# Optimization experiments

Measured on AMD Instinct MI355X. Metric: run time of the kernel, lower is better.

Reference implementation:

```python
import jax, jax.numpy as jnp
import numpy as np

TOP_K = 2
LN_EPS = 1e-5
GATE_EPS = 1e-6


def setup_inputs() -> dict:
    key = jax.random.key(0)
    ks = jax.random.split(key, 5)
    B, D, E, H, O = 16384, 1200, 8, 1024, 1
    x = jax.random.normal(ks[0], (B, D), dtype=jnp.float32)
    w_gate = jax.random.normal(ks[1], (D, E), dtype=jnp.float32) * 0.05
    W1 = jax.random.normal(ks[2], (E, D, H), dtype=jnp.float32) * (1.0 / np.sqrt(D))
    b1 = jnp.zeros((E, H), dtype=jnp.float32)
    g1 = jnp.ones((E, H), dtype=jnp.float32)   # LayerNorm weight
    be1 = jnp.zeros((E, H), dtype=jnp.float32)  # LayerNorm bias
    W2 = jax.random.normal(ks[3], (E, H, O), dtype=jnp.float32) * (1.0 / np.sqrt(H))
    b2 = jnp.zeros((E, O), dtype=jnp.float32)
    return {"x": x, "w_gate": w_gate, "W1": W1, "b1": b1, "g1": g1, "be1": be1, "W2": W2, "b2": b2}


def reference(x, w_gate, W1, b1, g1, be1, W2, b2):
    B = x.shape[0]
    # --- top-k gating (eval mode: no noise) ---
    probs = jax.nn.softmax(x @ w_gate, axis=1)                 # [B, E]
    top_vals, top_idx = jax.lax.top_k(probs, TOP_K)            # [B, k]
    top_gates = top_vals / (jnp.sum(top_vals, axis=1, keepdims=True) + GATE_EPS)
    gates = jnp.zeros_like(probs).at[jnp.arange(B)[:, None], top_idx].set(top_gates)  # [B, E]
    # --- per-expert MLP (computed densely for all experts; gates zero out non-selected) ---
    h = jnp.einsum('bd,edh->beh', x, W1) + b1                  # [B, E, H]
    mu = jnp.mean(h, axis=-1, keepdims=True)
    var = jnp.var(h, axis=-1, keepdims=True)
    h = (h - mu) * jax.lax.rsqrt(var + LN_EPS) * g1 + be1      # LayerNorm
    h = jax.nn.relu(h)
    out = jax.nn.sigmoid(jnp.einsum('beh,eho->beo', h, W2) + b2)  # [B, E, O]
    # --- scatter/combine: weighted sum over experts ---
    y = jnp.einsum('be,beo->bo', gates, out)                   # [B, O]
    return y
```

## Files before the change

### kernel.cpp

```cpp
#include <hip/hip_runtime.h>
#include <hip/hip_bf16.h>
#include <stdint.h>

#define B_ROWS 16384
#define D_IN   1200
#define D_PAD  1216
#define N_EXP  8
#define H_DIM  1024
#define R_CAP  4608
#define CAP    36864
#define N_RT   288
#define LN_EPS 1e-5f
#define GATE_EPS 1e-6f
#define CNT_STRIDE 16

#define O_CNT    0
#define O_PROWC  512
#define O_PGATEC 147968
#define O_XBF    295424
#define O_W1T    40143744
#define O_HBUF   60066688

#define GATING_BLOCKS (B_ROWS / 16)
#define W1T_BLOCKS    (19 * 16 * 8)
#define PREP_BLOCKS   (GATING_BLOCKS + 1 + W1T_BLOCKS)

#define NT        (D_PAD / 32)

typedef short bf16x8 __attribute__((ext_vector_type(8)));
typedef short short8 __attribute__((ext_vector_type(8)));
typedef short short4v __attribute__((ext_vector_type(4)));
typedef float f32x4 __attribute__((ext_vector_type(4)));

__device__ __forceinline__ void load_lds16(const void* gptr, void* ldsptr) {
    __builtin_amdgcn_global_load_lds(
        (__attribute__((address_space(1))) void*)const_cast<void*>(gptr),
        (__attribute__((address_space(3))) void*)ldsptr, 16, 0, 0);
}

__device__ __forceinline__ short4v pack_bf16x4(float4 a) {
    union { short4v v; __hip_bfloat16 h[4]; } u;
    u.h[0] = __float2bfloat16(a.x); u.h[1] = __float2bfloat16(a.y);
    u.h[2] = __float2bfloat16(a.z); u.h[3] = __float2bfloat16(a.w);
    return u.v;
}

__global__ __launch_bounds__(256) void prep_kernel(
    const float* __restrict__ x, const float* __restrict__ wg,
    int* __restrict__ cnt, int* __restrict__ pairRowC, float* __restrict__ pairGateC,
    __hip_bfloat16* __restrict__ xbf, float* __restrict__ y,
    const float* __restrict__ W1, __hip_bfloat16* __restrict__ w1t)
{
    __shared__ int lcnt[N_EXP];
    __shared__ int base[N_EXP];
    __shared__ float tile[2][32][33];
    int bx = blockIdx.x;
    int tid = threadIdx.x;

    if (bx > GATING_BLOCKS) {
        int b = bx - GATING_BLOCKS - 1;
        int d0 = (b % 19) * 64;
        int h0 = ((b / 19) % 16) * 64;
        int e = b / (19 * 16);
        const float* src = W1 + (long)e * D_IN * H_DIM;

        int hs = tid & 15;
        int dr = tid >> 4;
#pragma unroll
        for (int s = 0; s < 4; ++s) {
            int dl = dr + 16 * s;
            int d = d0 + dl;
            float4 v = (d < D_IN)
                ? ((const float4*)(src + (long)d * H_DIM + h0))[hs]
                : (float4){0.f, 0.f, 0.f, 0.f};
            int drl = dl & 31;
            int hl = hs * 4;
            int Th = hl >> 5;
            int hh = hl & 31;
            tile[Th][drl][hh + 0] = v.x;
            tile[Th][drl][hh + 1] = v.y;
            tile[Th][drl][hh + 2] = v.z;
            tile[Th][drl][hh + 3] = v.w;
            if (s == 1) {
                __syncthreads();
                int T2 = tid >> 7, rr = tid & 127;
                int hl2 = rr >> 2, dseg = rr & 3;
                float f[8];
#pragma unroll
                for (int jj = 0; jj < 8; ++jj) f[jj] = tile[T2][dseg * 8 + jj][hl2];
                union { short8 v8; __hip_bfloat16 hh8[8]; } u;
#pragma unroll
                for (int jj = 0; jj < 8; ++jj) u.hh8[jj] = __float2bfloat16(f[jj]);
                int h = h0 + T2 * 32 + hl2;
                ((short8*)(w1t + (long)e * H_DIM * D_PAD + (long)h * D_PAD + d0))[dseg] = u.v8;
                __syncthreads();
            }
        }
        __syncthreads();
        {
            int T2 = tid >> 7, rr = tid & 127;
            int hl2 = rr >> 2, dseg = rr & 3;
            float f[8];
#pragma unroll
            for (int jj = 0; jj < 8; ++jj) f[jj] = tile[T2][dseg * 8 + jj][hl2];
            union { short8 v8; __hip_bfloat16 hh8[8]; } u;
#pragma unroll
            for (int jj = 0; jj < 8; ++jj) u.hh8[jj] = __float2bfloat16(f[jj]);
            int h = h0 + T2 * 32 + hl2;
            ((short8*)(w1t + (long)e * H_DIM * D_PAD + (long)h * D_PAD + d0 + 32))[dseg] = u.v8;
        }
        return;
    }

    if (bx == GATING_BLOCKS) {
        short8* xrow = (short8*)(xbf + (long)B_ROWS * D_PAD);
        if (tid < 152) xrow[tid] = (short8){0, 0, 0, 0, 0, 0, 0, 0};
        return;
    }

    if (tid < N_EXP) lcnt[tid] = 0;
    if (tid < 16) y[bx * 16 + tid] = 0.f;
    __syncthreads();

    int widx = tid >> 6;
    int lane = tid & 63;
    int rowbase = bx * 16 + widx * 4;
    const float* xw = x + (long)rowbase * D_IN;

    float acc[4][8];
#pragma unroll
    for (int r = 0; r < 4; ++r)
#pragma unroll
        for (int e = 0; e < N_EXP; ++e) acc[r][e] = 0.f;

    for (int i = lane; i < 304; i += 64) {
        if (i < 300) {
            const float4* wv4 = (const float4*)(wg + (long)i * 32);
            float4 w0 = wv4[0], w1v = wv4[1], w2 = wv4[2], w3 = wv4[3],
                   w4 = wv4[4], w5 = wv4[5], w6 = wv4[6], w7 = wv4[7];
#pragma unroll
            for (int r = 0; r < 4; ++r) {
                float4 xv = ((const float4*)(xw + (long)r * D_IN))[i];
                acc[r][0] += xv.x * w0.x + xv.y * w2.x + xv.z * w4.x + xv.w * w6.x;
                acc[r][1] += xv.x * w0.y + xv.y * w2.y + xv.z * w4.y + xv.w * w6.y;
                acc[r][2] += xv.x * w0.z + xv.y * w2.z + xv.z * w4.z + xv.w * w6.z;
                acc[r][3] += xv.x * w0.w + xv.y * w2.w + xv.z * w4.w + xv.w * w6.w;
                acc[r][4] += xv.x * w1v.x + xv.y * w3.x + xv.z * w5.x + xv.w * w7.x;
                acc[r][5] += xv.x * w1v.y + xv.y * w3.y + xv.z * w5.y + xv.w * w7.y;
                acc[r][6] += xv.x * w1v.z + xv.y * w3.z + xv.z * w5.z + xv.w * w7.z;
                acc[r][7] += xv.x * w1v.w + xv.y * w3.w + xv.z * w5.w + xv.w * w7.w;
                ((short4v*)(xbf + (long)(rowbase + r) * D_PAD))[i] = pack_bf16x4(xv);
            }
        } else {
#pragma unroll
            for (int r = 0; r < 4; ++r)
                ((short4v*)(xbf + (long)(rowbase + r) * D_PAD))[i] = (short4v){0, 0, 0, 0};
        }
    }

#pragma unroll
    for (int r = 0; r < 4; ++r)
#pragma unroll
        for (int e = 0; e < N_EXP; ++e) {
            float v = acc[r][e];
#pragma unroll
            for (int off = 32; off > 0; off >>= 1) v += __shfl_xor(v, off, 64);
            acc[r][e] = v;
        }

    float my[N_EXP];
#pragma unroll
    for (int e = 0; e < N_EXP; ++e) my[e] = acc[0][e];
#pragma unroll
    for (int r = 1; r < 4; ++r)
#pragma unroll
        for (int e = 0; e < N_EXP; ++e)
            if (lane == r) my[e] = acc[r][e];

    int i0 = 0, i1 = 1, s0 = 0, s1 = 0;
    float g0 = 0.f, g1 = 0.f;
    if (lane < 4) {
        float m = my[0];
#pragma unroll
        for (int e = 1; e < N_EXP; ++e) m = fmaxf(m, my[e]);
        float p[N_EXP], s = 0.f;
#pragma unroll
        for (int e = 0; e < N_EXP; ++e) { p[e] = expf(my[e] - m); s += p[e]; }
#pragma unroll
        for (int e = 1; e < N_EXP; ++e) if (p[e] > p[i0]) i0 = e;
        i1 = (i0 == 0) ? 1 : 0;
#pragma unroll
        for (int e = 0; e < N_EXP; ++e) if (e != i0 && p[e] > p[i1]) i1 = e;
        float v0 = p[i0] / s, v1 = p[i1] / s;
        float inv = 1.f / (v0 + v1 + GATE_EPS);
        g0 = v0 * inv; g1 = v1 * inv;
        s0 = atomicAdd(&lcnt[i0], 1);
        s1 = atomicAdd(&lcnt[i1], 1);
    }
    __syncthreads();
    if (tid < N_EXP) base[tid] = atomicAdd(&cnt[tid * CNT_STRIDE], lcnt[tid]);
    __syncthreads();
    if (lane < 4) {
        int row = rowbase + lane;
        int p0 = i0 * R_CAP + base[i0] + s0;
        pairRowC[p0] = row; pairGateC[p0] = g0;
        int p1 = i1 * R_CAP + base[i1] + s1;
        pairRowC[p1] = row; pairGateC[p1] = g1;
    }
}

__global__ __launch_bounds__(256) void gemm_kernel(
    const __hip_bfloat16* __restrict__ xbf, const __hip_bfloat16* __restrict__ w1t,
    const float* __restrict__ b1, const int* __restrict__ cnt,
    const int* __restrict__ pairRowC,
    __hip_bfloat16* __restrict__ hbuf)
{
    int bi = blockIdx.x;
    int xcd = bi & 7;
    int j = bi >> 3;
    int col0 = (j & 7) << 7;
    int rt = xcd * 36 + (j >> 3);
    int row0 = rt << 7;
    int e = xcd;
    int cnt_e = cnt[e * CNT_STRIDE];
    if (row0 - e * R_CAP >= cnt_e) return;

    __shared__ short lA[128 * 32];
    __shared__ short lB[128 * 32];

    int t = threadIdx.x;
    int lane = t & 63, w = t >> 6;
    int wm = (w >> 1) * 64, wn = (w & 1) * 64;
    int l15 = lane & 15, quad = lane >> 4;
    int qsw = quad ^ ((l15 >> 1) & 3);

    f32x4 acc[4][4];
#pragma unroll
    for (int i = 0; i < 4; ++i)
#pragma unroll
        for (int j2 = 0; j2 < 4; ++j2) acc[i][j2] = (f32x4){0.f, 0.f, 0.f, 0.f};

    int r1 = t >> 2, seg = t & 3;
    int sw = seg ^ ((r1 >> 1) & 3);
    int ridx1 = pairRowC[row0 + r1];
    int ridx2 = pairRowC[row0 + 64 + r1];
    ridx1 = ((unsigned)ridx1 > B_ROWS) ? B_ROWS : ridx1;
    ridx2 = ((unsigned)ridx2 > B_ROWS) ? B_ROWS : ridx2;
    const __hip_bfloat16* Arow1 = xbf + (long)ridx1 * D_PAD + sw * 8;
    const __hip_bfloat16* Arow2 = xbf + (long)ridx2 * D_PAD + sw * 8;
    const __hip_bfloat16* Bb = w1t + (long)e * H_DIM * D_PAD + (long)col0 * D_PAD;
    const __hip_bfloat16* Brow1 = Bb + (long)r1 * D_PAD + sw * 8;
    const __hip_bfloat16* Brow2 = Bb + (long)(r1 + 64) * D_PAD + sw * 8;
    char* lAc = (char*)lA;
    char* lBc = (char*)lB;

    for (int kt = 0; kt < NT; ++kt) {
        __syncthreads();
        int k0 = kt * 32;
        load_lds16(Arow1 + k0, lAc + t * 16);
        load_lds16(Arow2 + k0, lAc + t * 16 + 4096);
        load_lds16(Brow1 + k0, lBc + t * 16);
        load_lds16(Brow2 + k0, lBc + t * 16 + 4096);
        __syncthreads();

        bf16x8 af[4], bfr[4];
#pragma unroll
        for (int i = 0; i < 4; ++i)
            af[i] = *(const bf16x8*)(lAc + (wm + i * 16 + l15) * 64 + qsw * 16);
#pragma unroll
        for (int j2 = 0; j2 < 4; ++j2)
            bfr[j2] = *(const bf16x8*)(lBc + (wn + j2 * 16 + l15) * 64 + qsw * 16);
#pragma unroll
        for (int i = 0; i < 4; ++i)
#pragma unroll
            for (int j2 = 0; j2 < 4; ++j2)
                acc[i][j2] = __builtin_amdgcn_mfma_f32_16x16x32_bf16(af[i], bfr[j2], acc[i][j2], 0, 0, 0);
    }

#pragma unroll
    for (int i = 0; i < 4; ++i) {
        int lr = wm + i * 16 + quad * 4;
#pragma unroll
        for (int j2 = 0; j2 < 4; ++j2) {
            int gc = col0 + wn + j2 * 16 + l15;
            float bias = b1[e * H_DIM + gc];
#pragma unroll
            for (int r = 0; r < 4; ++r) {
                float v = acc[i][j2][r] + bias;
                hbuf[(long)(row0 + lr + r) * H_DIM + gc] = __float2bfloat16(v);
            }
        }
    }
}

__global__ __launch_bounds__(256) void ln_head_kernel(
    const __hip_bfloat16* __restrict__ hbuf, const int* __restrict__ cnt,
    const int* __restrict__ pairRowC, const float* __restrict__ pairGateC,
    const float* __restrict__ g1, const float* __restrict__ be1,
    const float* __restrict__ W2, const float* __restrict__ b2,
    float* __restrict__ y)
{
    int tid = threadIdx.x;
    int p = blockIdx.x * 4 + (tid >> 6);
    int e = p / R_CAP;
    int slot = p - e * R_CAP;
    if (slot >= cnt[e * CNT_STRIDE]) return;

    int lane = tid & 63;
    int row = pairRowC[p];
    float gate = pairGateC[p];
    const short4v* hr = (const short4v*)(hbuf + (long)p * H_DIM);

    float v[16];
    float sum = 0.f, sumsq = 0.f;
#pragma unroll
    for (int k = 0; k < 4; ++k) {
        union { short4v s; __hip_bfloat16 h[4]; } hv;
        hv.s = hr[lane + k * 64];
#pragma unroll
        for (int j = 0; j < 4; ++j) {
            float f = __bfloat162float(hv.h[j]);
            v[k * 4 + j] = f;
            sum += f;
            sumsq += f * f;
        }
    }
#pragma unroll
    for (int off = 32; off > 0; off >>= 1) {
        sum += __shfl_xor(sum, off, 64);
        sumsq += __shfl_xor(sumsq, off, 64);
    }
    float mu = sum * (1.f / H_DIM);
    float var = sumsq * (1.f / H_DIM) - mu * mu;
    float rstd = rsqrtf(var + LN_EPS);

    float z = 0.f;
#pragma unroll
    for (int k = 0; k < 4; ++k) {
        float4 gv = ((const float4*)(g1 + e * H_DIM))[lane + k * 64];
        float4 bv = ((const float4*)(be1 + e * H_DIM))[lane + k * 64];
        float4 wv = ((const float4*)(W2 + e * H_DIM))[lane + k * 64];
        z += fmaxf((v[k*4+0] - mu) * rstd * gv.x + bv.x, 0.f) * wv.x;
        z += fmaxf((v[k*4+1] - mu) * rstd * gv.y + bv.y, 0.f) * wv.y;
        z += fmaxf((v[k*4+2] - mu) * rstd * gv.z + bv.z, 0.f) * wv.z;
        z += fmaxf((v[k*4+3] - mu) * rstd * gv.w + bv.w, 0.f) * wv.w;
    }
#pragma unroll
    for (int off = 32; off > 0; off >>= 1) z += __shfl_xor(z, off, 64);
    if (lane == 0) {
        float zt = z + b2[e];
        float o = 1.f / (1.f + expf(-zt));
        atomicAdd(&y[row], gate * o);
    }
}

extern "C" void kernel_launch(void* const* d_in, const int* in_sizes, int n_in,
                              void* d_out, int out_size, void* d_ws, size_t ws_size,
                              hipStream_t stream)
{
    const float* x   = (const float*)d_in[0];
    const float* wg  = (const float*)d_in[1];
    const float* W1  = (const float*)d_in[2];
    const float* b1  = (const float*)d_in[3];
    const float* g1  = (const float*)d_in[4];
    const float* be1 = (const float*)d_in[5];
    const float* W2  = (const float*)d_in[6];
    const float* b2  = (const float*)d_in[7];
    float* y = (float*)d_out;

    char* ws = (char*)d_ws;
    int*   cnt       = (int*)(ws + O_CNT);
    int*   pairRowC  = (int*)(ws + O_PROWC);
    float* pairGateC = (float*)(ws + O_PGATEC);
    __hip_bfloat16* xbf  = (__hip_bfloat16*)(ws + O_XBF);
    __hip_bfloat16* w1t  = (__hip_bfloat16*)(ws + O_W1T);
    __hip_bfloat16* hbuf = (__hip_bfloat16*)(ws + O_HBUF);

    hipMemsetAsync(cnt, 0, 512, stream);

    prep_kernel<<<PREP_BLOCKS, 256, 0, stream>>>(x, wg, cnt, pairRowC, pairGateC,
                                                 xbf, y, W1, w1t);
    gemm_kernel<<<N_RT * 8, 256, 0, stream>>>(xbf, w1t, b1, cnt, pairRowC, hbuf);
    ln_head_kernel<<<CAP / 4, 256, 0, stream>>>(hbuf, cnt, pairRowC, pairGateC,
                                                g1, be1, W2, b2, y);
}
```

Baseline: 293.5 us.

## Fuse LayerNorm head into GEMM via last-column-block completion counters

Removes the separate ln_head kernel. Each GEMM block bumps a per-row-tile byte counter packed into the zeroed cnt region, and the block that finishes last of the 8 column tiles runs the LayerNorm, ReLU, W2 dot, sigmoid and gated accumulation for that 128-row tile. This saves a kernel launch and lets the LN pass read hbuf while it is likely still in cache. In exchange, the LN work is serialized within one block per tile (32 rows per wave), which can lengthen the tail, and it relies on threadfence ordering for correctness.

Result: slower. 510.7 us (+74.0%).

```diff
diff --git a/kernel.cpp b/kernel.cpp
--- a/kernel.cpp
+++ b/kernel.cpp
@@ -43,6 +43,10 @@
     u.h[0] = __float2bfloat16(a.x); u.h[1] = __float2bfloat16(a.y);
     u.h[2] = __float2bfloat16(a.z); u.h[3] = __float2bfloat16(a.w);
     return u.v;
+}
+
+__device__ __forceinline__ int tile_ctr_idx(int word) {
+    return (word / 15) * 16 + 1 + (word % 15);
 }
 
 __global__ __launch_bounds__(256) void prep_kernel(
@@ -211,9 +215,12 @@
 
 __global__ __launch_bounds__(256) void gemm_kernel(
     const __hip_bfloat16* __restrict__ xbf, const __hip_bfloat16* __restrict__ w1t,
-    const float* __restrict__ b1, const int* __restrict__ cnt,
-    const int* __restrict__ pairRowC,
-    __hip_bfloat16* __restrict__ hbuf)
+    const float* __restrict__ b1, int* __restrict__ cnt,
+    const int* __restrict__ pairRowC, const float* __restrict__ pairGateC,
+    __hip_bfloat16* __restrict__ hbuf,
+    const float* __restrict__ g1, const float* __restrict__ be1,
+    const float* __restrict__ W2, const float* __restrict__ b2,
+    float* __restrict__ y)
 {
     int bi = blockIdx.x;
     int xcd = bi & 7;
@@ -227,6 +234,7 @@
 
     __shared__ short lA[128 * 32];
     __shared__ short lB[128 * 32];
+    __shared__ int doLN;
 
     int t = threadIdx.x;
     int lane = t & 63, w = t >> 6;
@@ -291,66 +299,70 @@
             }
         }
     }
-}
-
-__global__ __launch_bounds__(256) void ln_head_kernel(
-    const __hip_bfloat16* __restrict__ hbuf, const int* __restrict__ cnt,
-    const int* __restrict__ pairRowC, const float* __restrict__ pairGateC,
-    const float* __restrict__ g1, const float* __restrict__ be1,
-    const float* __restrict__ W2, const float* __restrict__ b2,
-    float* __restrict__ y)
-{
-    int tid = threadIdx.x;
-    int p = blockIdx.x * 4 + (tid >> 6);
-    int e = p / R_CAP;
-    int slot = p - e * R_CAP;
-    if (slot >= cnt[e * CNT_STRIDE]) return;
-
-    int lane = tid & 63;
-    int row = pairRowC[p];
-    float gate = pairGateC[p];
-    const short4v* hr = (const short4v*)(hbuf + (long)p * H_DIM);
-
-    float v[16];
-    float sum = 0.f, sumsq = 0.f;
-#pragma unroll
-    for (int k = 0; k < 4; ++k) {
-        union { short4v s; __hip_bfloat16 h[4]; } hv;
-        hv.s = hr[lane + k * 64];
-#pragma unroll
-        for (int j = 0; j < 4; ++j) {
-            float f = __bfloat162float(hv.h[j]);
-            v[k * 4 + j] = f;
-            sum += f;
-            sumsq += f * f;
-        }
-    }
-#pragma unroll
-    for (int off = 32; off > 0; off >>= 1) {
-        sum += __shfl_xor(sum, off, 64);
-        sumsq += __shfl_xor(sumsq, off, 64);
-    }
-    float mu = sum * (1.f / H_DIM);
-    float var = sumsq * (1.f / H_DIM) - mu * mu;
-    float rstd = rsqrtf(var + LN_EPS);
-
-    float z = 0.f;
-#pragma unroll
-    for (int k = 0; k < 4; ++k) {
-        float4 gv = ((const float4*)(g1 + e * H_DIM))[lane + k * 64];
-        float4 bv = ((const float4*)(be1 + e * H_DIM))[lane + k * 64];
-        float4 wv = ((const float4*)(W2 + e * H_DIM))[lane + k * 64];
-        z += fmaxf((v[k*4+0] - mu) * rstd * gv.x + bv.x, 0.f) * wv.x;
-        z += fmaxf((v[k*4+1] - mu) * rstd * gv.y + bv.y, 0.f) * wv.y;
-        z += fmaxf((v[k*4+2] - mu) * rstd * gv.z + bv.z, 0.f) * wv.z;
-        z += fmaxf((v[k*4+3] - mu) * rstd * gv.w + bv.w, 0.f) * wv.w;
-    }
-#pragma unroll
-    for (int off = 32; off > 0; off >>= 1) z += __shfl_xor(z, off, 64);
-    if (lane == 0) {
-        float zt = z + b2[e];
-        float o = 1.f / (1.f + expf(-zt));
-        atomicAdd(&y[row], gate * o);
+
+    __syncthreads();
+    if (t == 0) {
+        __threadfence();
+        int wordIdx = tile_ctr_idx(rt >> 2);
+        int shift = (rt & 3) * 8;
+        int old = atomicAdd(&cnt[wordIdx], 1 << shift);
+        doLN = (((old >> shift) & 255) == 7);
+    }
+    __syncthreads();
+    if (!doLN) return;
+
+    __threadfence();
+    {
+        int wv = t >> 6;
+        for (int rl = 0; rl < 32; ++rl) {
+            int p = row0 + wv * 32 + rl;
+            if (p - e * R_CAP >= cnt_e) continue;
+            int row = pairRowC[p];
+            float gate = pairGateC[p];
+            const short4v* hr = (const short4v*)(hbuf + (long)p * H_DIM);
+
+            float v[16];
+            float sum = 0.f, sumsq = 0.f;
+#pragma unroll
+            for (int k = 0; k < 4; ++k) {
+                union { short4v s; __hip_bfloat16 h[4]; } hv;
+                hv.s = hr[lane + k * 64];
+#pragma unroll
+                for (int jj = 0; jj < 4; ++jj) {
+                    float f = __bfloat162float(hv.h[jj]);
+                    v[k * 4 + jj] = f;
+                    sum += f;
+                    sumsq += f * f;
+                }
+            }
+#pragma unroll
+            for (int off = 32; off > 0; off >>= 1) {
+                sum += __shfl_xor(sum, off, 64);
+                sumsq += __shfl_xor(sumsq, off, 64);
+            }
+            float mu = sum * (1.f / H_DIM);
+            float var = sumsq * (1.f / H_DIM) - mu * mu;
+            float rstd = rsqrtf(var + LN_EPS);
+
+            float z = 0.f;
+#pragma unroll
+            for (int k = 0; k < 4; ++k) {
+                float4 gv = ((const float4*)(g1 + e * H_DIM))[lane + k * 64];
+                float4 bv = ((const float4*)(be1 + e * H_DIM))[lane + k * 64];
+                float4 wv2 = ((const float4*)(W2 + e * H_DIM))[lane + k * 64];
+                z += fmaxf((v[k*4+0] - mu) * rstd * gv.x + bv.x, 0.f) * wv2.x;
+                z += fmaxf((v[k*4+1] - mu) * rstd * gv.y + bv.y, 0.f) * wv2.y;
+                z += fmaxf((v[k*4+2] - mu) * rstd * gv.z + bv.z, 0.f) * wv2.z;
+                z += fmaxf((v[k*4+3] - mu) * rstd * gv.w + bv.w, 0.f) * wv2.w;
+            }
+#pragma unroll
+            for (int off = 32; off > 0; off >>= 1) z += __shfl_xor(z, off, 64);
+            if (lane == 0) {
+                float zt = z + b2[e];
+                float o = 1.f / (1.f + expf(-zt));
+                atomicAdd(&y[row], gate * o);
+            }
+        }
     }
 }
 
@@ -380,7 +392,6 @@
 
     prep_kernel<<<PREP_BLOCKS, 256, 0, stream>>>(x, wg, cnt, pairRowC, pairGateC,
                                                  xbf, y, W1, w1t);
-    gemm_kernel<<<N_RT * 8, 256, 0, stream>>>(xbf, w1t, b1, cnt, pairRowC, hbuf);
-    ln_head_kernel<<<CAP / 4, 256, 0, stream>>>(hbuf, cnt, pairRowC, pairGateC,
-                                                g1, be1, W2, b2, y);
-}
+    gemm_kernel<<<N_RT * 8, 256, 0, stream>>>(xbf, w1t, b1, cnt, pairRowC, pairGateC,
+                                              hbuf, g1, be1, W2, b2, y);
+}
```
